# Kernel tuning notes

Hardware: AMD Instinct MI355X
Metric: run time of the kernel (lower is better)

## Reference

```python
import jax, jax.numpy as jnp
import numpy as np

B, N, F, O = 4, 4096, 64, 64


def setup_inputs() -> dict:
    key = jax.random.key(0)
    k0, k1, k2, k3, k4 = jax.random.split(key, 5)
    x = jax.random.normal(k0, (B, N, F), dtype=jnp.float32)
    # adj_transform: Linear(2F -> 1): weight (2F,), bias scalar
    adj_w = jax.random.normal(k1, (2 * F,), dtype=jnp.float32) * (1.0 / np.sqrt(2 * F))
    adj_b = jax.random.normal(k2, (), dtype=jnp.float32)
    # GCN weight: xavier_normal_ over (F, O)
    weight = jax.random.normal(k3, (F, O), dtype=jnp.float32) * np.sqrt(2.0 / (F + O))
    bias = jax.random.normal(k4, (O,), dtype=jnp.float32)
    return {"x": x, "adj_w": adj_w, "adj_b": adj_b, "weight": weight, "bias": bias}


def reference(x, adj_w, adj_b, weight, bias):
    f = x.shape[-1]
    # Original: tmp[b,i,j] = x[b,j]; adj[b,i,j] = Linear(cat(x[b,j], x[b,i]))
    # = x[b,j]\u00b7adj_w[:F] + x[b,i]\u00b7adj_w[F:] + adj_b  (exact decomposition,
    # avoids materializing the (B,N,N,2F) concat tensor)
    s_col = jnp.einsum('bnf,f->bn', x, adj_w[:f])   # contributes along j
    s_row = jnp.einsum('bnf,f->bn', x, adj_w[f:])   # contributes along i
    adj = s_row[:, :, None] + s_col[:, None, :] + adj_b  # (B, N, N)
    # symmetric degree normalization with clamp(min=1)
    deg_inv_sqrt = jnp.clip(adj.sum(axis=-1), 1.0, None) ** -0.5  # (B, N)
    adj = deg_inv_sqrt[:, :, None] * adj * deg_inv_sqrt[:, None, :]
    out = jnp.einsum('bij,bjo->bio', adj, x @ weight) + bias
    return jax.nn.relu(out)
```

## Files before the change

kernel.cpp:

```cpp
#include <hip/hip_runtime.h>

#define Bq 4
#define Nq 4096
#define Fq 64
#define Oq 64
#define NBLK 256
#define TOKA 0x1B7F3A29u
#define TOKB 0x4E95C3D1u

__global__ __launch_bounds__(256) void gcn_fused(
    const float* __restrict__ x, const float* __restrict__ adj_w,
    const float* __restrict__ adj_bp, const float* __restrict__ weight,
    const float* __restrict__ bias, float* __restrict__ out,
    unsigned* __restrict__ tokA, unsigned* __restrict__ tokB,
    float* __restrict__ scs_slot, float* __restrict__ pxd,
    float* __restrict__ pxsd) {
  const int t = threadIdx.x;
  const int blk = blockIdx.x;
  const int batch = blk >> 6;
  const float adj_b = adj_bp[0];

  __shared__ float ls_row[64], ls_col[64], ld[64], lsd[64];
  __shared__ float red[2][16][64];
  __shared__ float redc[2][2][64];
  __shared__ float xdl[64], xsdl[64], ul[64], vl[64];
  __shared__ float s_scs;

  {
    const int g = t >> 2;
    const int l = t & 3;
    const int r = blk * 64 + g;
    const float4* xr = reinterpret_cast<const float4*>(x + (size_t)r * Fq);
    const float4* w0 = reinterpret_cast<const float4*>(adj_w);
    const float4* w1 = reinterpret_cast<const float4*>(adj_w + Fq);
    float sc = 0.f, sr = 0.f;
#pragma unroll
    for (int k = 0; k < 4; ++k) {
      const int idx = k * 4 + l;
      float4 xv = xr[idx];
      float4 wa = w0[idx];
      float4 wb = w1[idx];
      sc += xv.x * wa.x + xv.y * wa.y + xv.z * wa.z + xv.w * wa.w;
      sr += xv.x * wb.x + xv.y * wb.y + xv.z * wb.z + xv.w * wb.w;
    }
    sc += __shfl_xor(sc, 1);
    sc += __shfl_xor(sc, 2);
    sr += __shfl_xor(sr, 1);
    sr += __shfl_xor(sr, 2);
    if (l == 0) {
      ls_col[g] = sc;
      ls_row[g] = sr;
    }
  }
  __syncthreads();
  if (t < 64) {
    float val = ls_col[t];
#pragma unroll
    for (int m = 1; m < 64; m <<= 1) val += __shfl_xor(val, m);
    if (t == 0)
      __hip_atomic_store(&scs_slot[blk], val, __ATOMIC_RELAXED,
                         __HIP_MEMORY_SCOPE_AGENT);
  }

  const int fq = t & 15;
  const int jsub = t >> 4;
  const float4* x4 =
      reinterpret_cast<const float4*>(x) + (size_t)blk * 64 * 16 + fq;
  float4 xv0 = x4[(jsub + 0) * 16];
  float4 xv1 = x4[(jsub + 16) * 16];
  float4 xv2 = x4[(jsub + 32) * 16];
  float4 xv3 = x4[(jsub + 48) * 16];

  __syncthreads();
  if (t == 0) {
    asm volatile("s_waitcnt vmcnt(0)" ::: "memory");
    __hip_atomic_store(&tokA[blk], TOKA, __ATOMIC_RELAXED,
                       __HIP_MEMORY_SCOPE_AGENT);
  }
  if (t < 64) {
    while (__hip_atomic_load(&tokA[batch * 64 + t], __ATOMIC_RELAXED,
                             __HIP_MEMORY_SCOPE_AGENT) != TOKA) {
      __builtin_amdgcn_s_sleep(1);
    }
    float v = __hip_atomic_load(&scs_slot[batch * 64 + t], __ATOMIC_RELAXED,
                                __HIP_MEMORY_SCOPE_AGENT);
#pragma unroll
    for (int m = 1; m < 64; m <<= 1) v += __shfl_xor(v, m);
    if (t == 0) s_scs = v;
  }
  __syncthreads();

  const float scs = s_scs;
  if (t < 64) {
    float dg = rsqrtf(fmaxf(fmaf((float)Nq, ls_row[t] + adj_b, scs), 1.0f));
    ld[t] = dg;
    lsd[t] = ls_col[t] * dg;
  }
  __syncthreads();
  {
    float4 axd = {0.f, 0.f, 0.f, 0.f};
    float4 axsd = {0.f, 0.f, 0.f, 0.f};
    const float4 xv[4] = {xv0, xv1, xv2, xv3};
#pragma unroll
    for (int k = 0; k < 4; ++k) {
      const int j = jsub + k * 16;
      const float dj = ld[j];
      const float sdj = lsd[j];
      axd.x = fmaf(dj, xv[k].x, axd.x);
      axd.y = fmaf(dj, xv[k].y, axd.y);
      axd.z = fmaf(dj, xv[k].z, axd.z);
      axd.w = fmaf(dj, xv[k].w, axd.w);
      axsd.x = fmaf(sdj, xv[k].x, axsd.x);
      axsd.y = fmaf(sdj, xv[k].y, axsd.y);
      axsd.z = fmaf(sdj, xv[k].z, axsd.z);
      axsd.w = fmaf(sdj, xv[k].w, axsd.w);
    }
    *reinterpret_cast<float4*>(&red[0][jsub][fq * 4]) = axd;
    *reinterpret_cast<float4*>(&red[1][jsub][fq * 4]) = axsd;
  }
  __syncthreads();
  if (t < 64) {
    float s = 0.f;
#pragma unroll
    for (int c = 0; c < 16; ++c) s += red[0][c][t];
    __hip_atomic_store(&pxd[blk * 64 + t], s, __ATOMIC_RELAXED,
                       __HIP_MEMORY_SCOPE_AGENT);
  } else if (t < 128) {
    const int f = t & 63;
    float s = 0.f;
#pragma unroll
    for (int c = 0; c < 16; ++c) s += red[1][c][f];
    __hip_atomic_store(&pxsd[blk * 64 + f], s, __ATOMIC_RELAXED,
                       __HIP_MEMORY_SCOPE_AGENT);
  }

  __syncthreads();
  if (t == 0) {
    asm volatile("s_waitcnt vmcnt(0)" ::: "memory");
    __hip_atomic_store(&tokB[blk], TOKB, __ATOMIC_RELAXED,
                       __HIP_MEMORY_SCOPE_AGENT);
  }
  if (t < 64) {
    while (__hip_atomic_load(&tokB[batch * 64 + t], __ATOMIC_RELAXED,
                             __HIP_MEMORY_SCOPE_AGENT) != TOKB) {
      __builtin_amdgcn_s_sleep(1);
    }
  }
  __syncthreads();

  {
    const int q = t >> 7;
    const int h = (t >> 6) & 1;
    const int f = t & 63;
    float* src = (q ? pxsd : pxd) + (size_t)batch * 64 * 64 + h * 32 * 64 + f;
    float s = 0.f;
#pragma unroll
    for (int c = 0; c < 32; ++c)
      s += __hip_atomic_load(src + c * 64, __ATOMIC_RELAXED,
                             __HIP_MEMORY_SCOPE_AGENT);
    redc[q][h][f] = s;
  }
  __syncthreads();
  if (t < 128) {
    const int f = t & 63;
    if (t < 64)
      xdl[f] = redc[0][0][f] + redc[0][1][f];
    else
      xsdl[f] = redc[1][0][f] + redc[1][1][f];
  }
  __syncthreads();
  if (t < 128) {
    const int o = t & 63;
    const float* src = (t < 64) ? xdl : xsdl;
    float acc = 0.f;
#pragma unroll
    for (int f = 0; f < Fq; ++f) acc = fmaf(src[f], weight[f * Oq + o], acc);
    if (t < 64)
      ul[o] = acc;
    else
      vl[o] = acc;
  }
  __syncthreads();
  {
    const int oq = t & 15;
    const int o0 = oq * 4;
    const float4 bv = reinterpret_cast<const float4*>(bias)[oq];
#pragma unroll
    for (int pass = 0; pass < 4; ++pass) {
      const int g = pass * 16 + (t >> 4);
      const int r = blk * 64 + g;
      const float di = ld[g];
      const float a = di * (ls_row[g] + adj_b);
      float4 rr;
      rr.x = fmaxf(0.f, fmaf(a, ul[o0 + 0], fmaf(di, vl[o0 + 0], bv.x)));
      rr.y = fmaxf(0.f, fmaf(a, ul[o0 + 1], fmaf(di, vl[o0 + 1], bv.y)));
      rr.z = fmaxf(0.f, fmaf(a, ul[o0 + 2], fmaf(di, vl[o0 + 2], bv.z)));
      rr.w = fmaxf(0.f, fmaf(a, ul[o0 + 3], fmaf(di, vl[o0 + 3], bv.w)));
      reinterpret_cast<float4*>(out + (size_t)r * Oq)[oq] = rr;
    }
  }
}

extern "C" void kernel_launch(void* const* d_in, const int* in_sizes, int n_in,
                              void* d_out, int out_size, void* d_ws,
                              size_t ws_size, hipStream_t stream) {
  const float* x = (const float*)d_in[0];
  const float* adj_w = (const float*)d_in[1];
  const float* adj_b = (const float*)d_in[2];
  const float* weight = (const float*)d_in[3];
  const float* bias = (const float*)d_in[4];
  float* out = (float*)d_out;

  float* ws = (float*)d_ws;
  unsigned* tokA = (unsigned*)ws;
  unsigned* tokB = (unsigned*)(ws + 256);
  float* scs_slot = ws + 512;
  float* pxd = ws + 768;
  float* pxsd = pxd + 256 * 64;

  hipLaunchKernelGGL(gcn_fused, dim3(NBLK), dim3(256), 0, stream, x, adj_w,
                     adj_b, weight, bias, out, tokA, tokB, scs_slot, pxd,
                     pxsd);
}
```

Before: 70.98 us.

## Pack token with column sum in one 64-bit flag and widen cross-block reduction loads

Combines the first grid-barrier token and the per-block column-sum value into a single 64-bit atomic store, so one store and one poll replace a flag store, a slot store, the waitcnt and an extra load. It drops the s_sleep in both spin loops to cut wake-up latency. The cross-block partial-sum gather now uses eight vectorized dwordx4 loads per thread with sc0 sc1 cache bits, followed by a shared-memory tree reduction, in place of 32 serial scalar atomic loads. The trade-offs are busier polling traffic and reliance on inline asm for coherence, and the eight-way reduction tree changes the floating-point summation order.

```diff
diff --git a/kernel.cpp b/kernel.cpp
--- a/kernel.cpp
+++ b/kernel.cpp
@@ -8,13 +8,19 @@
 #define TOKA 0x1B7F3A29u
 #define TOKB 0x4E95C3D1u
 
+typedef unsigned long long u64;
+
+#define LLC_LOAD4(dst, addr)                                        \
+  asm volatile("global_load_dwordx4 %0, %1, off sc0 sc1"            \
+               : "=&v"(dst)                                         \
+               : "v"(addr))
+
 __global__ __launch_bounds__(256) void gcn_fused(
     const float* __restrict__ x, const float* __restrict__ adj_w,
     const float* __restrict__ adj_bp, const float* __restrict__ weight,
     const float* __restrict__ bias, float* __restrict__ out,
-    unsigned* __restrict__ tokA, unsigned* __restrict__ tokB,
-    float* __restrict__ scs_slot, float* __restrict__ pxd,
-    float* __restrict__ pxsd) {
+    u64* __restrict__ tokA, unsigned* __restrict__ tokB,
+    float* __restrict__ pxd, float* __restrict__ pxsd) {
   const int t = threadIdx.x;
   const int blk = blockIdx.x;
   const int batch = blk >> 6;
@@ -22,7 +28,7 @@
 
   __shared__ float ls_row[64], ls_col[64], ld[64], lsd[64];
   __shared__ float red[2][16][64];
-  __shared__ float redc[2][2][64];
+  __shared__ float redc[2][8][64];
   __shared__ float xdl[64], xsdl[64], ul[64], vl[64];
   __shared__ float s_scs;
 
@@ -57,10 +63,13 @@
     float val = ls_col[t];
 #pragma unroll
     for (int m = 1; m < 64; m <<= 1) val += __shfl_xor(val, m);
-    if (t == 0)
-      __hip_atomic_store(&scs_slot[blk], val, __ATOMIC_RELAXED,
+    if (t == 0) {
+      u64 pk = ((u64)TOKA << 32) | (u64)__float_as_uint(val);
+      __hip_atomic_store(&tokA[blk], pk, __ATOMIC_RELAXED,
                          __HIP_MEMORY_SCOPE_AGENT);
-  }
+    }
+  }
+  asm volatile("" ::: "memory");
 
   const int fq = t & 15;
   const int jsub = t >> 4;
@@ -71,19 +80,13 @@
   float4 xv2 = x4[(jsub + 32) * 16];
   float4 xv3 = x4[(jsub + 48) * 16];
 
-  __syncthreads();
-  if (t == 0) {
-    asm volatile("s_waitcnt vmcnt(0)" ::: "memory");
-    __hip_atomic_store(&tokA[blk], TOKA, __ATOMIC_RELAXED,
-                       __HIP_MEMORY_SCOPE_AGENT);
-  }
-  if (t < 64) {
-    while (__hip_atomic_load(&tokA[batch * 64 + t], __ATOMIC_RELAXED,
-                             __HIP_MEMORY_SCOPE_AGENT) != TOKA) {
-      __builtin_amdgcn_s_sleep(1);
-    }
-    float v = __hip_atomic_load(&scs_slot[batch * 64 + t], __ATOMIC_RELAXED,
-                                __HIP_MEMORY_SCOPE_AGENT);
+  if (t < 64) {
+    u64 pk;
+    do {
+      pk = __hip_atomic_load(&tokA[batch * 64 + t], __ATOMIC_RELAXED,
+                             __HIP_MEMORY_SCOPE_AGENT);
+    } while ((unsigned)(pk >> 32) != TOKA);
+    float v = __uint_as_float((unsigned)pk);
 #pragma unroll
     for (int m = 1; m < 64; m <<= 1) v += __shfl_xor(v, m);
     if (t == 0) s_scs = v;
@@ -143,30 +146,47 @@
   if (t < 64) {
     while (__hip_atomic_load(&tokB[batch * 64 + t], __ATOMIC_RELAXED,
                              __HIP_MEMORY_SCOPE_AGENT) != TOKB) {
-      __builtin_amdgcn_s_sleep(1);
-    }
-  }
-  __syncthreads();
+    }
+  }
+  __syncthreads();
+  asm volatile("" ::: "memory");
 
   {
     const int q = t >> 7;
-    const int h = (t >> 6) & 1;
-    const int f = t & 63;
-    float* src = (q ? pxsd : pxd) + (size_t)batch * 64 * 64 + h * 32 * 64 + f;
-    float s = 0.f;
-#pragma unroll
-    for (int c = 0; c < 32; ++c)
-      s += __hip_atomic_load(src + c * 64, __ATOMIC_RELAXED,
-                             __HIP_MEMORY_SCOPE_AGENT);
-    redc[q][h][f] = s;
+    const int c8 = (t >> 4) & 7;
+    const int fqd = t & 15;
+    const float* src = (q ? pxsd : pxd) + (size_t)batch * 64 * 64 +
+                       (size_t)c8 * 8 * 64 + fqd * 4;
+    float4 r0, r1, r2, r3, r4, r5, r6, r7;
+    LLC_LOAD4(r0, src + 0 * 64);
+    LLC_LOAD4(r1, src + 1 * 64);
+    LLC_LOAD4(r2, src + 2 * 64);
+    LLC_LOAD4(r3, src + 3 * 64);
+    LLC_LOAD4(r4, src + 4 * 64);
+    LLC_LOAD4(r5, src + 5 * 64);
+    LLC_LOAD4(r6, src + 6 * 64);
+    LLC_LOAD4(r7, src + 7 * 64);
+    asm volatile("s_waitcnt vmcnt(0)" ::: "memory");
+    __builtin_amdgcn_sched_barrier(0);
+    float4 s;
+    s.x = ((r0.x + r1.x) + (r2.x + r3.x)) + ((r4.x + r5.x) + (r6.x + r7.x));
+    s.y = ((r0.y + r1.y) + (r2.y + r3.y)) + ((r4.y + r5.y) + (r6.y + r7.y));
+    s.z = ((r0.z + r1.z) + (r2.z + r3.z)) + ((r4.z + r5.z) + (r6.z + r7.z));
+    s.w = ((r0.w + r1.w) + (r2.w + r3.w)) + ((r4.w + r5.w) + (r6.w + r7.w));
+    *reinterpret_cast<float4*>(&redc[q][c8][fqd * 4]) = s;
   }
   __syncthreads();
   if (t < 128) {
     const int f = t & 63;
-    if (t < 64)
-      xdl[f] = redc[0][0][f] + redc[0][1][f];
+    const int q = t >> 6;
+    float a = ((redc[q][0][f] + redc[q][1][f]) +
+               (redc[q][2][f] + redc[q][3][f])) +
+              ((redc[q][4][f] + redc[q][5][f]) +
+               (redc[q][6][f] + redc[q][7][f]));
+    if (q == 0)
+      xdl[f] = a;
     else
-      xsdl[f] = redc[1][0][f] + redc[1][1][f];
+      xsdl[f] = a;
   }
   __syncthreads();
   if (t < 128) {
@@ -212,13 +232,11 @@
   float* out = (float*)d_out;
 
   float* ws = (float*)d_ws;
-  unsigned* tokA = (unsigned*)ws;
-  unsigned* tokB = (unsigned*)(ws + 256);
-  float* scs_slot = ws + 512;
+  u64* tokA = (u64*)ws;
+  unsigned* tokB = (unsigned*)(ws + 512);
   float* pxd = ws + 768;
   float* pxsd = pxd + 256 * 64;
 
   hipLaunchKernelGGL(gcn_fused, dim3(NBLK), dim3(256), 0, stream, x, adj_w,
-                     adj_b, weight, bias, out, tokA, tokB, scs_slot, pxd,
-                     pxsd);
+                     adj_b, weight, bias, out, tokA, tokB, pxd, pxsd);
 }
```

Result: faster. 69.33 us (-2.3%).
